# Kernel tuning notes

Hardware: AMD Instinct MI355X
Metric: run time of the kernel (lower is better)

Reference implementation:

```python
import jax, jax.numpy as jnp
import numpy as np

B = 8192        # number of contexts
T_SIDE = 10     # num_cx_tokens_per_side
NT = 10         # cx_max_num_types
V_TOK = 5000
V_TYP = 5000
D_TOK = 128
D_TYP = 32
H = 32          # hole_rnn_layer_size
D_IN = D_TOK + D_TYP  # 160


def setup_inputs() -> dict:
    key = jax.random.key(0)
    ks = jax.random.split(key, 32)
    def n(k, shape, scale=1.0):
        return jax.random.normal(k, shape, dtype=jnp.float32) * scale
    def rmask(k, shape):
        m = jax.random.randint(k, shape, 0, 2).astype(bool)
        return m.at[:, :, 0].set(True)  # first type slot always valid (as in data loader)
    inp = {}
    inp['tokens_before'] = jax.random.randint(ks[0], (B, T_SIDE), 0, V_TOK, dtype=jnp.int32)
    inp['types_before'] = jax.random.randint(ks[1], (B, T_SIDE, NT), 0, V_TYP, dtype=jnp.int32)
    inp['mask_before'] = rmask(ks[2], (B, T_SIDE, NT))
    inp['tokens_after'] = jax.random.randint(ks[3], (B, T_SIDE), 0, V_TOK, dtype=jnp.int32)
    inp['types_after'] = jax.random.randint(ks[4], (B, T_SIDE, NT), 0, V_TYP, dtype=jnp.int32)
    inp['mask_after'] = rmask(ks[5], (B, T_SIDE, NT))
    inp['token_embeddings'] = n(ks[6], (V_TOK, D_TOK))
    inp['type_embeddings'] = n(ks[7], (V_TYP, D_TYP))
    inp['hole_representation'] = n(ks[8], (1, 1, D_IN))
    # GRU kernels (TF GRUCell layout): gate kernel [(in+h), 2h], candidate [(in+h), h]
    i = 9
    for layer, din in ((0, D_IN), (1, 2 * H)):
        for d in ('fw', 'bw'):
            inp[f'gk_{d}{layer}'] = n(ks[i], (din + H, 2 * H), 0.1); i += 1
            inp[f'gb_{d}{layer}'] = jnp.zeros((2 * H,), jnp.float32)
            inp[f'ck_{d}{layer}'] = n(ks[i], (din + H, H), 0.1); i += 1
            inp[f'cb_{d}{layer}'] = jnp.zeros((H,), jnp.float32)
    return inp


def _embed(tokens, types, mask, tok_emb, typ_emb):
    te = tok_emb[tokens]                                 # [B,T,128]
    ty = typ_emb[types]                                  # [B,T,NT,32]
    ty = ty + (1.0 - mask[..., None].astype(jnp.float32)) * -1000.0
    ty = jnp.max(ty, axis=2)                             # masked max over types -> [B,T,32]
    return jnp.concatenate([te, ty], axis=-1)            # [B,T,160]


def _gru(x_seq, gk, gb, ck, cb):
    # x_seq: [T,B,D]; TF GRUCell math: r,u = sigmoid([x,h]Wg+bg); c = tanh([x, r*h]Wc+bc); h' = u*h+(1-u)*c
    h0 = jnp.zeros((x_seq.shape[1], cb.shape[0]), x_seq.dtype)
    def step(h, x):
        ru = jax.nn.sigmoid(jnp.concatenate([x, h], -1) @ gk + gb)
        r, u = jnp.split(ru, 2, axis=-1)
        c = jnp.tanh(jnp.concatenate([x, r * h], -1) @ ck + cb)
        h_new = u * h + (1.0 - u) * c
        return h_new, h_new
    _, ys = jax.lax.scan(step, h0, x_seq)
    return ys                                            # [T,B,H]


def _bidir(x_seq, pf, pb):
    fw = _gru(x_seq, *pf)
    bw = jnp.flip(_gru(jnp.flip(x_seq, 0), *pb), 0)
    return jnp.concatenate([fw, bw], axis=-1)            # [T,B,2H]


def reference(tokens_before, types_before, mask_before, tokens_after, types_after, mask_after,
              token_embeddings, type_embeddings, hole_representation,
              gk_fw0, gb_fw0, ck_fw0, cb_fw0, gk_bw0, gb_bw0, ck_bw0, cb_bw0,
              gk_fw1, gb_fw1, ck_fw1, cb_fw1, gk_bw1, gb_bw1, ck_bw1, cb_bw1):
    before = _embed(tokens_before, types_before, mask_before, token_embeddings, type_embeddings)
    after = _embed(tokens_after, types_after, mask_after, token_embeddings, type_embeddings)
    nb = before.shape[0]
    hole = jnp.broadcast_to(hole_representation, (nb, 1, D_IN))
    seq = jnp.concatenate([before, hole, after], axis=1)  # [B,21,160]
    x = jnp.transpose(seq, (1, 0, 2))                     # [T,B,D]
    y0 = _bidir(x, (gk_fw0, gb_fw0, ck_fw0, cb_fw0), (gk_bw0, gb_bw0, ck_bw0, cb_bw0))
    y1 = _bidir(y0, (gk_fw1, gb_fw1, ck_fw1, cb_fw1), (gk_bw1, gb_bw1, ck_bw1, cb_bw1))
    return jnp.transpose(y1, (1, 0, 2))                   # [B,21,64]
```

## Files before the change

kernel.cpp:

```cpp
#include <hip/hip_runtime.h>


typedef __attribute__((ext_vector_type(8))) short short8;
typedef __attribute__((ext_vector_type(8))) __bf16 bf16x8;
typedef __attribute__((ext_vector_type(4))) float f32x4;
typedef unsigned short ushort_t;

#define U_TOKEMB  0
#define U_TYPEMB  640000
#define U_HOLE    800000
#define U_GKFW0   800160
#define U_GBFW0   812448
#define U_CKFW0   812512
#define U_CBFW0   818656
#define U_GKBW0   818688
#define U_GBBW0   830976
#define U_CKBW0   831040
#define U_CBBW0   837184
#define U_GKFW1   837216
#define U_GBFW1   843360
#define U_CKFW1   843424
#define U_CBFW1   846496
#define U_GKBW1   846528
#define U_GBBW1   852672
#define U_CKBW1   852736
#define U_CBBW1   855808

#define Y0A_OFF   (4u << 20)
#define TYPF_OFF  (25u << 20)

__device__ __forceinline__ float bf2f(unsigned int u) {
  union { unsigned int i; float f; } v; v.i = u << 16; return v.f;
}
__device__ __forceinline__ unsigned short f2bf(float f) {
  unsigned int u = __float_as_uint(f);
  u += 0x7fffu + ((u >> 16) & 1u);
  return (unsigned short)(u >> 16);
}
__device__ __forceinline__ f32x4 mfma16(short8 a, short8 b, f32x4 c) {
  return __builtin_amdgcn_mfma_f32_16x16x32_bf16(
      __builtin_bit_cast(bf16x8, a), __builtin_bit_cast(bf16x8, b), c, 0, 0, 0);
}
__device__ __forceinline__ float sgm(float x) {
  x = fminf(fmaxf(x, -30.f), 30.f);
  return __fdividef(1.f, 1.f + __expf(-x));
}
__device__ __forceinline__ float tnh(float x) {
  x = fminf(fmaxf(x, -15.f), 15.f);
  float e = __expf(2.f * x);
  return (e - 1.f) * __fdividef(1.f, e + 1.f);
}

__global__ void k0_detect(const ushort_t* __restrict__ probe_f,
                          const unsigned* __restrict__ probe_m,
                          const unsigned* __restrict__ probe_t,
                          int* __restrict__ flags) {
  const int lane = threadIdx.x;
  int cnt = 0;
#pragma unroll
  for (int i = 0; i < 4; ++i) {
    unsigned e = ((unsigned)probe_f[lane + i * 64] >> 7) & 0xffu;
    if (e == 0u || (e >= 112u && e <= 134u)) cnt++;
  }
#pragma unroll
  for (int off = 32; off > 0; off >>= 1) cnt += __shfl_down(cnt, off, 64);
  const unsigned v = probe_m[lane];
  const unsigned long long bytelike =
      __ballot((v > 1u) && (v != 0x3F800000u) && ((v & 0xFEFEFEFEu) == 0u));
  const unsigned tv = probe_t[lane];
  const unsigned long long tlooksTypes =
      __ballot(!(tv == 0u || tv == 1u || tv == 0x3F800000u));
  if (lane == 0) {
    flags[0] = (cnt < 205) ? 1 : 0;
    flags[1] = bytelike ? 1 : 0;
    flags[2] = tlooksTypes ? 0 : 1;
  }
}

struct Cvt19 { const void* src[19]; int len[19]; int dst[19]; };

__global__ void kcvt(Cvt19 a, ushort_t* __restrict__ cvt, const int* __restrict__ flags) {
  const int fp32 = flags[0];
  int gid = blockIdx.x * blockDim.x + threadIdx.x;
#pragma unroll 1
  for (int s = 0; s < 19; ++s) {
    if (gid < a.len[s]) {
      cvt[a.dst[s] + gid] = fp32 ? f2bf(((const float*)a.src[s])[gid])
                                 : ((const ushort_t*)a.src[s])[gid];
      return;
    }
    gid -= a.len[s];
  }
}

__global__ __launch_bounds__(256) void ktypmax(
    const void* __restrict__ slot_tb, const void* __restrict__ slot_mb,
    const void* __restrict__ slot_ta, const void* __restrict__ slot_ma,
    const ushort_t* __restrict__ cvt, uint4* __restrict__ typf,
    const int* __restrict__ flags) {
  const int wv = threadIdx.x >> 6;
  const int lane = threadIdx.x & 63;
  const int q = lane >> 4, nl = lane & 15;
  const int job = blockIdx.x * 4 + wv;
  const int st = job >> 9;
  const int btile = job & 511;
  const int side = (st >= 10) ? 1 : 0;
  const int ts = st - side * 10;
  const int b = btile * 16 + nl;
  const int sw = flags[2];
  const int bytem = flags[1];
  const int* tys = side ? (const int*)(sw ? slot_ma : slot_ta)
                        : (const int*)(sw ? slot_mb : slot_tb);
  const void* msk = side ? (sw ? slot_ta : slot_ma)
                         : (sw ? slot_tb : slot_mb);
  const int base = (b * 10 + ts) * 10;
  float mx[8];
#pragma unroll
  for (int j = 0; j < 8; ++j) mx[j] = -1e30f;
#pragma unroll
  for (int nt = 0; nt < 10; ++nt) {
    const int ty = tys[base + nt];
    const bool mv = bytem ? (((const unsigned char*)msk)[base + nt] != 0)
                          : (((const unsigned*)msk)[base + nt] != 0u);
    const float pen = mv ? 0.f : -1000.f;
    uint4 e = *reinterpret_cast<const uint4*>(cvt + U_TYPEMB + (size_t)ty * 32 + q * 8);
    const unsigned w[4] = {e.x, e.y, e.z, e.w};
#pragma unroll
    for (int j2 = 0; j2 < 4; ++j2) {
      mx[2 * j2]     = fmaxf(mx[2 * j2],     bf2f(w[j2] & 0xffffu) + pen);
      mx[2 * j2 + 1] = fmaxf(mx[2 * j2 + 1], bf2f(w[j2] >> 16) + pen);
    }
  }
  short8 v;
#pragma unroll
  for (int j = 0; j < 8; ++j) v[j] = (short)f2bf(mx[j]);
  typf[(size_t)job * 64 + lane] = __builtin_bit_cast(uint4, v);
}

__device__ __forceinline__ void gatherX(
    int t, int btile, int lane,
    const int* __restrict__ tok_b, const int* __restrict__ tok_a,
    const ushort_t* __restrict__ cvt, const uint4* __restrict__ typf,
    short8 af[5]) {
  const int q = lane >> 4, nl = lane & 15;
  if (t == 10) {
#pragma unroll
    for (int kt = 0; kt < 5; ++kt)
      af[kt] = __builtin_bit_cast(short8,
          *reinterpret_cast<const uint4*>(cvt + U_HOLE + kt * 32 + q * 8));
    return;
  }
  const int ts = (t < 10) ? t : t - 11;
  const int side = (t < 10) ? 0 : 1;
  const int b = btile * 16 + nl;
  const int tok = (side ? tok_a : tok_b)[b * 10 + ts];
#pragma unroll
  for (int kt = 0; kt < 4; ++kt)
    af[kt] = __builtin_bit_cast(short8,
        *reinterpret_cast<const uint4*>(cvt + U_TOKEMB + (size_t)tok * 128 + kt * 32 + q * 8));
  af[4] = __builtin_bit_cast(short8,
      typf[((size_t)(side * 10 + ts) * 512 + btile) * 64 + lane]);
}

__global__ __launch_bounds__(256, 1) void krec0(
    const int* __restrict__ tok_b, const int* __restrict__ tok_a,
    const ushort_t* __restrict__ cvt, const uint4* __restrict__ typf,
    uint4* __restrict__ y0a) {
  __shared__ __align__(16) ushort_t hbuf[4][2][16 * 40];
  const int wv = threadIdx.x >> 6;
  const int lane = threadIdx.x & 63;
  const int q = lane >> 4, nl = lane & 15;
  const int job = blockIdx.x * 4 + wv;
  const int dir = job & 1, btile = job >> 1;

  const ushort_t* gk = cvt + (dir ? U_GKBW0 : U_GKFW0);
  const ushort_t* ck = cvt + (dir ? U_CKBW0 : U_CKFW0);
  const ushort_t* gb = cvt + (dir ? U_GBBW0 : U_GBFW0);
  const ushort_t* cb = cvt + (dir ? U_CBBW0 : U_CBFW0);

  short8 wg[5][4], wc[5][2], wgh[4], wch[2];
#pragma unroll
  for (int kt = 0; kt < 5; ++kt) {
#pragma unroll
    for (int tn = 0; tn < 4; ++tn) {
      short8 v;
#pragma unroll
      for (int j = 0; j < 8; ++j) v[j] = (short)gk[(kt * 32 + q * 8 + j) * 64 + tn * 16 + nl];
      wg[kt][tn] = v;
    }
#pragma unroll
    for (int tn = 0; tn < 2; ++tn) {
      short8 v;
#pragma unroll
      for (int j = 0; j < 8; ++j) v[j] = (short)ck[(kt * 32 + q * 8 + j) * 32 + tn * 16 + nl];
      wc[kt][tn] = v;
    }
  }
#pragma unroll
  for (int tn = 0; tn < 4; ++tn) {
    short8 v;
#pragma unroll
    for (int j = 0; j < 8; ++j) v[j] = (short)gk[(160 + q * 8 + j) * 64 + tn * 16 + nl];
    wgh[tn] = v;
  }
#pragma unroll
  for (int tn = 0; tn < 2; ++tn) {
    short8 v;
#pragma unroll
    for (int j = 0; j < 8; ++j) v[j] = (short)ck[(160 + q * 8 + j) * 32 + tn * 16 + nl];
    wch[tn] = v;
  }
  float gb4[4], cb4[2];
#pragma unroll
  for (int tn = 0; tn < 4; ++tn) gb4[tn] = bf2f((unsigned)gb[tn * 16 + nl]);
#pragma unroll
  for (int tn = 0; tn < 2; ++tn) cb4[tn] = bf2f((unsigned)cb[tn * 16 + nl]);

  f32x4 hc0 = {0.f, 0.f, 0.f, 0.f}, hc1 = {0.f, 0.f, 0.f, 0.f};
  short8 hA = {0, 0, 0, 0, 0, 0, 0, 0};
  ushort_t* hb0 = hbuf[wv][0];
  ushort_t* hb1 = hbuf[wv][1];

  short8 afc[5], afn[5];
  gatherX(dir ? 20 : 0, btile, lane, tok_b, tok_a, cvt, typf, afc);

  for (int s = 0; s < 21; ++s) {
    const int t = dir ? 20 - s : s;
    if (s < 20)
      gatherX(dir ? t - 1 : t + 1, btile, lane, tok_b, tok_a, cvt, typf, afn);

    f32x4 ru[4];
#pragma unroll
    for (int tn = 0; tn < 4; ++tn) {
      f32x4 acc = {gb4[tn], gb4[tn], gb4[tn], gb4[tn]};
#pragma unroll
      for (int kt = 0; kt < 5; ++kt) acc = mfma16(afc[kt], wg[kt][tn], acc);
      acc = mfma16(hA, wgh[tn], acc);
      ru[tn] = acc;
    }
#pragma unroll
    for (int tn = 0; tn < 4; ++tn)
#pragma unroll
      for (int r = 0; r < 4; ++r) ru[tn][r] = sgm(ru[tn][r]);

#pragma unroll
    for (int r = 0; r < 4; ++r) {
      hb0[(q * 4 + r) * 40 + nl]      = f2bf(ru[0][r] * hc0[r]);
      hb0[(q * 4 + r) * 40 + 16 + nl] = f2bf(ru[1][r] * hc1[r]);
    }
    short8 rhA = *reinterpret_cast<const short8*>(hb0 + nl * 40 + q * 8);

    f32x4 cc0 = {cb4[0], cb4[0], cb4[0], cb4[0]};
    f32x4 cc1 = {cb4[1], cb4[1], cb4[1], cb4[1]};
#pragma unroll
    for (int kt = 0; kt < 5; ++kt) {
      cc0 = mfma16(afc[kt], wc[kt][0], cc0);
      cc1 = mfma16(afc[kt], wc[kt][1], cc1);
    }
    cc0 = mfma16(rhA, wch[0], cc0);
    cc1 = mfma16(rhA, wch[1], cc1);
#pragma unroll
    for (int r = 0; r < 4; ++r) {
      const float c0 = tnh(cc0[r]), c1 = tnh(cc1[r]);
      const float u0 = ru[2][r], u1 = ru[3][r];
      hc0[r] = u0 * hc0[r] + (1.f - u0) * c0;
      hc1[r] = u1 * hc1[r] + (1.f - u1) * c1;
    }

#pragma unroll
    for (int r = 0; r < 4; ++r) {
      hb1[(q * 4 + r) * 40 + nl]      = f2bf(hc0[r]);
      hb1[(q * 4 + r) * 40 + 16 + nl] = f2bf(hc1[r]);
    }
    hA = *reinterpret_cast<const short8*>(hb1 + nl * 40 + q * 8);
    y0a[((size_t)(t * 512 + btile) * 2 + dir) * 64 + lane] = __builtin_bit_cast(uint4, hA);

    if (s < 20) {
#pragma unroll
      for (int kt = 0; kt < 5; ++kt) afc[kt] = afn[kt];
    }
  }
}

__global__ __launch_bounds__(256, 1) void k3b(
    const ushort_t* __restrict__ cvt, const uint4* __restrict__ y0a,
    float* __restrict__ out) {
  __shared__ __align__(16) ushort_t hbuf[4][2][16 * 40];
  const int wv = threadIdx.x >> 6;
  const int lane = threadIdx.x & 63;
  const int q = lane >> 4, nl = lane & 15;
  const int job = blockIdx.x * 4 + wv;
  const int dir = job & 1, btile = job >> 1;
  const ushort_t* gk = cvt + (dir ? U_GKBW1 : U_GKFW1);
  const ushort_t* ck = cvt + (dir ? U_CKBW1 : U_CKFW1);
  const ushort_t* gb = cvt + (dir ? U_GBBW1 : U_GBFW1);
  const ushort_t* cb = cvt + (dir ? U_CBBW1 : U_CBFW1);

  short8 wg[3][4], wc[3][2];
#pragma unroll
  for (int kt = 0; kt < 3; ++kt) {
#pragma unroll
    for (int tn = 0; tn < 4; ++tn) {
      short8 v;
#pragma unroll
      for (int j = 0; j < 8; ++j) v[j] = (short)gk[(kt * 32 + q * 8 + j) * 64 + tn * 16 + nl];
      wg[kt][tn] = v;
    }
#pragma unroll
    for (int tn = 0; tn < 2; ++tn) {
      short8 v;
#pragma unroll
      for (int j = 0; j < 8; ++j) v[j] = (short)ck[(kt * 32 + q * 8 + j) * 32 + tn * 16 + nl];
      wc[kt][tn] = v;
    }
  }
  float gb4[4], cb4[2];
#pragma unroll
  for (int tn = 0; tn < 4; ++tn) gb4[tn] = bf2f((unsigned)gb[tn * 16 + nl]);
#pragma unroll
  for (int tn = 0; tn < 2; ++tn) cb4[tn] = bf2f((unsigned)cb[tn * 16 + nl]);

  f32x4 hc0 = {0.f, 0.f, 0.f, 0.f}, hc1 = {0.f, 0.f, 0.f, 0.f};
  short8 hA = {0, 0, 0, 0, 0, 0, 0, 0};
  ushort_t* hb0 = hbuf[wv][0];
  ushort_t* hb1 = hbuf[wv][1];

  short8 ya0, ya1, yn0, yn1;
  {
    const int t0 = dir ? 20 : 0;
    ya0 = __builtin_bit_cast(short8, y0a[((size_t)(t0 * 512 + btile) * 2 + 0) * 64 + lane]);
    ya1 = __builtin_bit_cast(short8, y0a[((size_t)(t0 * 512 + btile) * 2 + 1) * 64 + lane]);
  }

  for (int s = 0; s < 21; ++s) {
    const int t = dir ? 20 - s : s;
    if (s < 20) {
      const int t2 = dir ? t - 1 : t + 1;
      yn0 = __builtin_bit_cast(short8, y0a[((size_t)(t2 * 512 + btile) * 2 + 0) * 64 + lane]);
      yn1 = __builtin_bit_cast(short8, y0a[((size_t)(t2 * 512 + btile) * 2 + 1) * 64 + lane]);
    }

    f32x4 ru[4];
#pragma unroll
    for (int tn = 0; tn < 4; ++tn) {
      f32x4 acc = {gb4[tn], gb4[tn], gb4[tn], gb4[tn]};
      acc = mfma16(ya0, wg[0][tn], acc);
      acc = mfma16(ya1, wg[1][tn], acc);
      acc = mfma16(hA,  wg[2][tn], acc);
      ru[tn] = acc;
    }
#pragma unroll
    for (int tn = 0; tn < 4; ++tn)
#pragma unroll
      for (int r = 0; r < 4; ++r) ru[tn][r] = sgm(ru[tn][r]);

#pragma unroll
    for (int r = 0; r < 4; ++r) {
      hb0[(q * 4 + r) * 40 + nl]      = f2bf(ru[0][r] * hc0[r]);
      hb0[(q * 4 + r) * 40 + 16 + nl] = f2bf(ru[1][r] * hc1[r]);
    }
    short8 rhA = *reinterpret_cast<const short8*>(hb0 + nl * 40 + q * 8);

    f32x4 cc0 = {cb4[0], cb4[0], cb4[0], cb4[0]};
    cc0 = mfma16(ya0, wc[0][0], cc0);
    cc0 = mfma16(ya1, wc[1][0], cc0);
    cc0 = mfma16(rhA, wc[2][0], cc0);
    f32x4 cc1 = {cb4[1], cb4[1], cb4[1], cb4[1]};
    cc1 = mfma16(ya0, wc[0][1], cc1);
    cc1 = mfma16(ya1, wc[1][1], cc1);
    cc1 = mfma16(rhA, wc[2][1], cc1);

#pragma unroll
    for (int r = 0; r < 4; ++r) {
      const float c0 = tnh(cc0[r]), c1 = tnh(cc1[r]);
      const float u0 = ru[2][r], u1 = ru[3][r];
      hc0[r] = u0 * hc0[r] + (1.f - u0) * c0;
      hc1[r] = u1 * hc1[r] + (1.f - u1) * c1;
    }

#pragma unroll
    for (int r = 0; r < 4; ++r) {
      hb1[(q * 4 + r) * 40 + nl]      = f2bf(hc0[r]);
      hb1[(q * 4 + r) * 40 + 16 + nl] = f2bf(hc1[r]);
    }
    hA = *reinterpret_cast<const short8*>(hb1 + nl * 40 + q * 8);

#pragma unroll
    for (int r = 0; r < 4; ++r) {
      const size_t o = ((size_t)(btile * 16 + q * 4 + r) * 21 + t) * 64 + dir * 32 + nl;
      out[o]      = hc0[r];
      out[o + 16] = hc1[r];
    }

    if (s < 20) { ya0 = yn0; ya1 = yn1; }
  }
}

extern "C" void kernel_launch(void* const* d_in, const int* in_sizes, int n_in,
                              void* d_out, int out_size, void* d_ws, size_t ws_size,
                              hipStream_t stream)
{
  const int* tok_b = (const int*)d_in[0];
  const void* slot_tb = d_in[1];
  const void* slot_mb = d_in[2];
  const int* tok_a = (const int*)d_in[3];
  const void* slot_ta = d_in[4];
  const void* slot_ma = d_in[5];

  int* flags = (int*)d_ws;
  ushort_t* cvt = (ushort_t*)((char*)d_ws + 64);
  uint4* y0a = (uint4*)((char*)d_ws + Y0A_OFF);
  uint4* typf = (uint4*)((char*)d_ws + TYPF_OFF);

  k0_detect<<<dim3(1), dim3(64), 0, stream>>>(
      (const ushort_t*)d_in[6], (const unsigned*)slot_mb, (const unsigned*)slot_tb,
      flags);

  static const int slen[19] = {640000, 160000, 160,
                               12288, 64, 6144, 32, 12288, 64, 6144, 32,
                               6144, 64, 3072, 32, 6144, 64, 3072, 32};
  static const int sdst[19] = {U_TOKEMB, U_TYPEMB, U_HOLE,
                               U_GKFW0, U_GBFW0, U_CKFW0, U_CBFW0,
                               U_GKBW0, U_GBBW0, U_CKBW0, U_CBBW0,
                               U_GKFW1, U_GBFW1, U_CKFW1, U_CBFW1,
                               U_GKBW1, U_GBBW1, U_CKBW1, U_CBBW1};
  Cvt19 a;
  int tot = 0;
  for (int i = 0; i < 19; ++i) {
    a.src[i] = d_in[6 + i]; a.len[i] = slen[i]; a.dst[i] = sdst[i]; tot += slen[i];
  }
  kcvt<<<dim3((tot + 255) / 256), dim3(256), 0, stream>>>(a, cvt, flags);

  ktypmax<<<dim3(2560), dim3(256), 0, stream>>>(
      slot_tb, slot_mb, slot_ta, slot_ma, cvt, typf, flags);

  krec0<<<dim3(256), dim3(256), 0, stream>>>(tok_b, tok_a, cvt, typf, y0a);

  k3b<<<dim3(256), dim3(256), 0, stream>>>(cvt, y0a, (float*)d_out);
}
```

Before: 212.3 us.

## Pre-swizzle GRU weights into MFMA fragments and pack bf16 hidden-state stores

Adds a small kernel that rearranges all GRU weight matrices once into per-lane MFMA fragment order. The recurrent kernels then load each fragment with a single 16-byte read instead of eight strided scalar gathers. The hidden-state LDS writes now use a packed bf16 conversion instruction and an interleaved column order, with the recurrent weight rows permuted to match. The sigmoid and tanh input clamps are removed and the exact division is replaced by the hardware reciprocal. This relies on the reciprocal of inf giving zero for saturation, and it adds one extra kernel launch.

```diff
diff --git a/kernel.cpp b/kernel.cpp
--- a/kernel.cpp
+++ b/kernel.cpp
@@ -28,6 +28,7 @@
 
 #define Y0A_OFF   (4u << 20)
 #define TYPF_OFF  (25u << 20)
+#define WF_OFF    (37u << 20)
 
 __device__ __forceinline__ float bf2f(unsigned int u) {
   union { unsigned int i; float f; } v; v.i = u << 16; return v.f;
@@ -37,19 +38,23 @@
   u += 0x7fffu + ((u >> 16) & 1u);
   return (unsigned short)(u >> 16);
 }
+__device__ __forceinline__ unsigned cvtpk(float a, float b) {
+  unsigned r;
+  asm("v_cvt_pk_bf16_f32 %0, %1, %2" : "=v"(r) : "v"(a), "v"(b));
+  return r;
+}
 __device__ __forceinline__ f32x4 mfma16(short8 a, short8 b, f32x4 c) {
   return __builtin_amdgcn_mfma_f32_16x16x32_bf16(
       __builtin_bit_cast(bf16x8, a), __builtin_bit_cast(bf16x8, b), c, 0, 0, 0);
 }
+__device__ __forceinline__ float frcp(float x) { return __builtin_amdgcn_rcpf(x); }
 __device__ __forceinline__ float sgm(float x) {
-  x = fminf(fmaxf(x, -30.f), 30.f);
-  return __fdividef(1.f, 1.f + __expf(-x));
+  return frcp(1.f + __expf(-x));
 }
 __device__ __forceinline__ float tnh(float x) {
-  x = fminf(fmaxf(x, -15.f), 15.f);
-  float e = __expf(2.f * x);
-  return (e - 1.f) * __fdividef(1.f, e + 1.f);
-}
+  return 1.f - 2.f * frcp(__expf(2.f * x) + 1.f);
+}
+__device__ __forceinline__ int PIk(int p) { return (p >> 1) + ((p & 1) << 4); }
 
 __global__ void k0_detect(const ushort_t* __restrict__ probe_f,
                           const unsigned* __restrict__ probe_m,
@@ -91,6 +96,41 @@
     }
     gid -= a.len[s];
   }
+}
+
+__global__ void kswz(const ushort_t* __restrict__ cvt, uint4* __restrict__ wf) {
+  const int id = blockIdx.x * blockDim.x + threadIdx.x;
+  if (id >= 108 * 64) return;
+  const int frag = id >> 6, lane = id & 63;
+  const int q = lane >> 4, nl = lane & 15;
+  const int layer = (frag >= 72) ? 1 : 0;
+  const int fr = layer ? frag - 72 : frag;
+  const int nper = layer ? 18 : 36;
+  const int d = fr / nper;
+  const int f = fr - d * nper;
+  const ushort_t* gk = layer ? (cvt + (d ? U_GKBW1 : U_GKFW1))
+                             : (cvt + (d ? U_GKBW0 : U_GKFW0));
+  const ushort_t* ck = layer ? (cvt + (d ? U_CKBW1 : U_CKFW1))
+                             : (cvt + (d ? U_CKBW0 : U_CKFW0));
+  const ushort_t* src; int row0, colw, coloff; bool perm;
+  if (!layer) {
+    if (f < 20)      { src = gk; row0 = (f >> 2) * 32; colw = 64; coloff = (f & 3) * 16; perm = false; }
+    else if (f < 30) { int g = f - 20; src = ck; row0 = (g >> 1) * 32; colw = 32; coloff = (g & 1) * 16; perm = false; }
+    else if (f < 34) { src = gk; row0 = 160; colw = 64; coloff = (f - 30) * 16; perm = true; }
+    else             { src = ck; row0 = 160; colw = 32; coloff = (f - 34) * 16; perm = true; }
+  } else {
+    perm = true;
+    if (f < 12)      { src = gk; row0 = (f >> 2) * 32; colw = 64; coloff = (f & 3) * 16; }
+    else             { int g = f - 12; src = ck; row0 = (g >> 1) * 32; colw = 32; coloff = (g & 1) * 16; }
+  }
+  short8 v;
+#pragma unroll
+  for (int j = 0; j < 8; ++j) {
+    const int p = q * 8 + j;
+    const int row = row0 + (perm ? PIk(p) : p);
+    v[j] = (short)src[row * colw + coloff + nl];
+  }
+  wf[frag * 64 + lane] = __builtin_bit_cast(uint4, v);
 }
 
 __global__ __launch_bounds__(256) void ktypmax(
@@ -164,8 +204,8 @@
 
 __global__ __launch_bounds__(256, 1) void krec0(
     const int* __restrict__ tok_b, const int* __restrict__ tok_a,
-    const ushort_t* __restrict__ cvt, const uint4* __restrict__ typf,
-    uint4* __restrict__ y0a) {
+    const ushort_t* __restrict__ cvt, const uint4* __restrict__ wf,
+    const uint4* __restrict__ typf, uint4* __restrict__ y0a) {
   __shared__ __align__(16) ushort_t hbuf[4][2][16 * 40];
   const int wv = threadIdx.x >> 6;
   const int lane = threadIdx.x & 63;
@@ -173,43 +213,26 @@
   const int job = blockIdx.x * 4 + wv;
   const int dir = job & 1, btile = job >> 1;
 
-  const ushort_t* gk = cvt + (dir ? U_GKBW0 : U_GKFW0);
-  const ushort_t* ck = cvt + (dir ? U_CKBW0 : U_CKFW0);
+  const uint4* wfL0 = wf + dir * 36 * 64;
+  short8 wg[5][4], wc[5][2], wgh[4], wch[2];
+#pragma unroll
+  for (int kt = 0; kt < 5; ++kt) {
+#pragma unroll
+    for (int tn = 0; tn < 4; ++tn)
+      wg[kt][tn] = __builtin_bit_cast(short8, wfL0[(kt * 4 + tn) * 64 + lane]);
+#pragma unroll
+    for (int tn = 0; tn < 2; ++tn)
+      wc[kt][tn] = __builtin_bit_cast(short8, wfL0[(20 + kt * 2 + tn) * 64 + lane]);
+  }
+#pragma unroll
+  for (int tn = 0; tn < 4; ++tn)
+    wgh[tn] = __builtin_bit_cast(short8, wfL0[(30 + tn) * 64 + lane]);
+#pragma unroll
+  for (int tn = 0; tn < 2; ++tn)
+    wch[tn] = __builtin_bit_cast(short8, wfL0[(34 + tn) * 64 + lane]);
+
   const ushort_t* gb = cvt + (dir ? U_GBBW0 : U_GBFW0);
   const ushort_t* cb = cvt + (dir ? U_CBBW0 : U_CBFW0);
-
-  short8 wg[5][4], wc[5][2], wgh[4], wch[2];
-#pragma unroll
-  for (int kt = 0; kt < 5; ++kt) {
-#pragma unroll
-    for (int tn = 0; tn < 4; ++tn) {
-      short8 v;
-#pragma unroll
-      for (int j = 0; j < 8; ++j) v[j] = (short)gk[(kt * 32 + q * 8 + j) * 64 + tn * 16 + nl];
-      wg[kt][tn] = v;
-    }
-#pragma unroll
-    for (int tn = 0; tn < 2; ++tn) {
-      short8 v;
-#pragma unroll
-      for (int j = 0; j < 8; ++j) v[j] = (short)ck[(kt * 32 + q * 8 + j) * 32 + tn * 16 + nl];
-      wc[kt][tn] = v;
-    }
-  }
-#pragma unroll
-  for (int tn = 0; tn < 4; ++tn) {
-    short8 v;
-#pragma unroll
-    for (int j = 0; j < 8; ++j) v[j] = (short)gk[(160 + q * 8 + j) * 64 + tn * 16 + nl];
-    wgh[tn] = v;
-  }
-#pragma unroll
-  for (int tn = 0; tn < 2; ++tn) {
-    short8 v;
-#pragma unroll
-    for (int j = 0; j < 8; ++j) v[j] = (short)ck[(160 + q * 8 + j) * 32 + tn * 16 + nl];
-    wch[tn] = v;
-  }
   float gb4[4], cb4[2];
 #pragma unroll
   for (int tn = 0; tn < 4; ++tn) gb4[tn] = bf2f((unsigned)gb[tn * 16 + nl]);
@@ -244,10 +267,9 @@
       for (int r = 0; r < 4; ++r) ru[tn][r] = sgm(ru[tn][r]);
 
 #pragma unroll
-    for (int r = 0; r < 4; ++r) {
-      hb0[(q * 4 + r) * 40 + nl]      = f2bf(ru[0][r] * hc0[r]);
-      hb0[(q * 4 + r) * 40 + 16 + nl] = f2bf(ru[1][r] * hc1[r]);
-    }
+    for (int r = 0; r < 4; ++r)
+      *reinterpret_cast<unsigned*>(hb0 + (q * 4 + r) * 40 + 2 * nl) =
+          cvtpk(ru[0][r] * hc0[r], ru[1][r] * hc1[r]);
     short8 rhA = *reinterpret_cast<const short8*>(hb0 + nl * 40 + q * 8);
 
     f32x4 cc0 = {cb4[0], cb4[0], cb4[0], cb4[0]};
@@ -268,10 +290,9 @@
     }
 
 #pragma unroll
-    for (int r = 0; r < 4; ++r) {
-      hb1[(q * 4 + r) * 40 + nl]      = f2bf(hc0[r]);
-      hb1[(q * 4 + r) * 40 + 16 + nl] = f2bf(hc1[r]);
-    }
+    for (int r = 0; r < 4; ++r)
+      *reinterpret_cast<unsigned*>(hb1 + (q * 4 + r) * 40 + 2 * nl) =
+          cvtpk(hc0[r], hc1[r]);
     hA = *reinterpret_cast<const short8*>(hb1 + nl * 40 + q * 8);
     y0a[((size_t)(t * 512 + btile) * 2 + dir) * 64 + lane] = __builtin_bit_cast(uint4, hA);
 
@@ -283,37 +304,28 @@
 }
 
 __global__ __launch_bounds__(256, 1) void k3b(
-    const ushort_t* __restrict__ cvt, const uint4* __restrict__ y0a,
-    float* __restrict__ out) {
+    const ushort_t* __restrict__ cvt, const uint4* __restrict__ wf,
+    const uint4* __restrict__ y0a, float* __restrict__ out) {
   __shared__ __align__(16) ushort_t hbuf[4][2][16 * 40];
   const int wv = threadIdx.x >> 6;
   const int lane = threadIdx.x & 63;
   const int q = lane >> 4, nl = lane & 15;
   const int job = blockIdx.x * 4 + wv;
   const int dir = job & 1, btile = job >> 1;
-  const ushort_t* gk = cvt + (dir ? U_GKBW1 : U_GKFW1);
-  const ushort_t* ck = cvt + (dir ? U_CKBW1 : U_CKFW1);
+
+  const uint4* wfL1 = wf + (72 + dir * 18) * 64;
+  short8 wg[3][4], wc[3][2];
+#pragma unroll
+  for (int kt = 0; kt < 3; ++kt) {
+#pragma unroll
+    for (int tn = 0; tn < 4; ++tn)
+      wg[kt][tn] = __builtin_bit_cast(short8, wfL1[(kt * 4 + tn) * 64 + lane]);
+#pragma unroll
+    for (int tn = 0; tn < 2; ++tn)
+      wc[kt][tn] = __builtin_bit_cast(short8, wfL1[(12 + kt * 2 + tn) * 64 + lane]);
+  }
   const ushort_t* gb = cvt + (dir ? U_GBBW1 : U_GBFW1);
   const ushort_t* cb = cvt + (dir ? U_CBBW1 : U_CBFW1);
-
-  short8 wg[3][4], wc[3][2];
-#pragma unroll
-  for (int kt = 0; kt < 3; ++kt) {
-#pragma unroll
-    for (int tn = 0; tn < 4; ++tn) {
-      short8 v;
-#pragma unroll
-      for (int j = 0; j < 8; ++j) v[j] = (short)gk[(kt * 32 + q * 8 + j) * 64 + tn * 16 + nl];
-      wg[kt][tn] = v;
-    }
-#pragma unroll
-    for (int tn = 0; tn < 2; ++tn) {
-      short8 v;
-#pragma unroll
-      for (int j = 0; j < 8; ++j) v[j] = (short)ck[(kt * 32 + q * 8 + j) * 32 + tn * 16 + nl];
-      wc[kt][tn] = v;
-    }
-  }
   float gb4[4], cb4[2];
 #pragma unroll
   for (int tn = 0; tn < 4; ++tn) gb4[tn] = bf2f((unsigned)gb[tn * 16 + nl]);
@@ -355,10 +367,9 @@
       for (int r = 0; r < 4; ++r) ru[tn][r] = sgm(ru[tn][r]);
 
 #pragma unroll
-    for (int r = 0; r < 4; ++r) {
-      hb0[(q * 4 + r) * 40 + nl]      = f2bf(ru[0][r] * hc0[r]);
-      hb0[(q * 4 + r) * 40 + 16 + nl] = f2bf(ru[1][r] * hc1[r]);
-    }
+    for (int r = 0; r < 4; ++r)
+      *reinterpret_cast<unsigned*>(hb0 + (q * 4 + r) * 40 + 2 * nl) =
+          cvtpk(ru[0][r] * hc0[r], ru[1][r] * hc1[r]);
     short8 rhA = *reinterpret_cast<const short8*>(hb0 + nl * 40 + q * 8);
 
     f32x4 cc0 = {cb4[0], cb4[0], cb4[0], cb4[0]};
@@ -379,10 +390,9 @@
     }
 
 #pragma unroll
-    for (int r = 0; r < 4; ++r) {
-      hb1[(q * 4 + r) * 40 + nl]      = f2bf(hc0[r]);
-      hb1[(q * 4 + r) * 40 + 16 + nl] = f2bf(hc1[r]);
-    }
+    for (int r = 0; r < 4; ++r)
+      *reinterpret_cast<unsigned*>(hb1 + (q * 4 + r) * 40 + 2 * nl) =
+          cvtpk(hc0[r], hc1[r]);
     hA = *reinterpret_cast<const short8*>(hb1 + nl * 40 + q * 8);
 
 #pragma unroll
@@ -411,6 +421,7 @@
   ushort_t* cvt = (ushort_t*)((char*)d_ws + 64);
   uint4* y0a = (uint4*)((char*)d_ws + Y0A_OFF);
   uint4* typf = (uint4*)((char*)d_ws + TYPF_OFF);
+  uint4* wf  = (uint4*)((char*)d_ws + WF_OFF);
 
   k0_detect<<<dim3(1), dim3(64), 0, stream>>>(
       (const ushort_t*)d_in[6], (const unsigned*)slot_mb, (const unsigned*)slot_tb,
@@ -431,10 +442,12 @@
   }
   kcvt<<<dim3((tot + 255) / 256), dim3(256), 0, stream>>>(a, cvt, flags);
 
+  kswz<<<dim3(27), dim3(256), 0, stream>>>(cvt, wf);
+
   ktypmax<<<dim3(2560), dim3(256), 0, stream>>>(
       slot_tb, slot_mb, slot_ta, slot_ma, cvt, typf, flags);
 
-  krec0<<<dim3(256), dim3(256), 0, stream>>>(tok_b, tok_a, cvt, typf, y0a);
-
-  k3b<<<dim3(256), dim3(256), 0, stream>>>(cvt, y0a, (float*)d_out);
-}
+  krec0<<<dim3(256), dim3(256), 0, stream>>>(tok_b, tok_a, cvt, wf, typf, y0a);
+
+  k3b<<<dim3(256), dim3(256), 0, stream>>>(cvt, wf, y0a, (float*)d_out);
+}
```

After: 188.1 us. -11.4%, faster.
